# Optimization experiments

Measured on AMD Instinct MI355X. Metric: run time of the kernel, lower is better.

## Reference

```python
import jax, jax.numpy as jnp
import numpy as np

N, E, D, H, B = 10000, 160000, 128, 1, 4
SLOPE = 0.01  # negative_slope from DeepQNet default


def gat_layer(x, node_state, src, dst, W, att_src, att_dst, Wns, bns, bias):
    # x: [N,D] or [B,N,D]; node_state: [B,N,1]
    xs = x + node_state @ Wns + bns              # [B,N,D]
    Bx, Nn = xs.shape[0], xs.shape[1]
    h = (xs @ W).reshape(Bx, Nn, H, D)           # [B,N,H,C]
    a_src = (h * att_src).sum(-1)                # [B,N,H]
    a_dst = (h * att_dst).sum(-1)                # [B,N,H]
    ae = a_src[:, src] + a_dst[:, dst]           # [B,Etot,H]
    ae = jnp.where(ae > 0, ae, SLOPE * ae)       # leaky_relu
    ae_t = jnp.moveaxis(ae, 1, 0)                # [Etot,B,H]
    m = jax.ops.segment_max(ae_t, dst, num_segments=Nn)   # [N,B,H]
    e = jnp.exp(ae_t - m[dst])
    s = jax.ops.segment_sum(e, dst, num_segments=Nn)
    alpha = e / s[dst]                           # [Etot,B,H]
    h_e = jnp.moveaxis(h, 1, 0)                  # [N,B,H,C]
    msg = alpha[..., None] * h_e[src]            # [Etot,B,H,C]
    out = jax.ops.segment_sum(msg, dst, num_segments=Nn)  # [N,B,H,C]
    out = jnp.moveaxis(out, 0, 1).mean(2) + bias # concat=False -> head mean
    return jax.nn.relu(out)


def setup_inputs() -> dict:
    key = jax.random.key(0)
    ks = jax.random.split(key, 16)
    edges = jax.random.randint(ks[0], (2, E), 0, N)
    loop = jnp.arange(N)
    edge_index = jnp.concatenate([edges, jnp.stack([loop, loop])], axis=1)  # add_self_loops
    state = jax.random.uniform(ks[1], (B, N), dtype=jnp.float32)
    strucEmb = jax.random.normal(ks[2], (N, D), dtype=jnp.float32) * 0.1
    s = 0.05
    return {
        "state": state,
        "strucEmb": strucEmb,
        "edge_index": edge_index,
        "gat_W": jax.random.normal(ks[3], (3, D, H * D), dtype=jnp.float32) * s,
        "gat_att_src": jax.random.normal(ks[4], (3, H, D), dtype=jnp.float32) * s,
        "gat_att_dst": jax.random.normal(ks[5], (3, H, D), dtype=jnp.float32) * s,
        "gat_Wns": jax.random.normal(ks[6], (3, 1, D), dtype=jnp.float32) * s,
        "gat_bns": jnp.zeros((3, D), jnp.float32),
        "gat_bias": jnp.zeros((3, D), jnp.float32),
        "W1": jax.random.normal(ks[7], (D, D), dtype=jnp.float32) * s,
        "b1": jnp.zeros((D,), jnp.float32),
        "W2": jax.random.normal(ks[8], (D, D), dtype=jnp.float32) * s,
        "b2": jnp.zeros((D,), jnp.float32),
        "W3": jax.random.normal(ks[9], (2 * D, 1), dtype=jnp.float32) * s,
        "b3": jnp.zeros((1,), jnp.float32),
    }


def reference(state, strucEmb, edge_index, gat_W, gat_att_src, gat_att_dst,
              gat_Wns, gat_bns, gat_bias, W1, b1, W2, b2, W3, b3):
    src, dst = edge_index[0], edge_index[1]
    rs = state.reshape(state.shape[0], N, 1)     # [B,N,1]
    x = strucEmb
    for l in range(3):
        x = gat_layer(x, rs, src, dst, gat_W[l], gat_att_src[l], gat_att_dst[l],
                      gat_Wns[l], gat_bns[l], gat_bias[l])
    state_emb = x.sum(1)                         # [B,D]
    beta_state = state_emb @ W1 + b1             # [B,D]
    beta_action = x @ W2 + b2                    # [B,N,D]  (is_for_learn=True path)
    expand_state = jnp.broadcast_to(beta_state[:, None, :], beta_action.shape)
    out = jax.nn.relu(jnp.concatenate([expand_state, beta_action], axis=2))
    return out @ W3 + b3                         # [B,N,1]
```

## Files before the change

kernel.cpp:

```cpp
#include <hip/hip_runtime.h>
#include <math.h>

#define N_NODES 10000
#define B_SZ 4
#define SLOPE 0.01f
#define BN (B_SZ * N_NODES)
#define PADK 136

typedef __attribute__((ext_vector_type(8))) short short8;
typedef __attribute__((ext_vector_type(4))) float float4v;

__device__ __forceinline__ unsigned short f2bf(float f) {
    unsigned u = __builtin_bit_cast(unsigned, f);
    u += 0x7fffu + ((u >> 16) & 1u);
    return (unsigned short)(u >> 16);
}
__device__ __forceinline__ float bf2f(unsigned short s) {
    unsigned u = ((unsigned)s) << 16;
    return __builtin_bit_cast(float, u);
}


__global__ __launch_bounds__(256) void init_kernel(int* deg, int* cursor, float* state_emb) {
    int i = blockIdx.x * 256 + threadIdx.x;
    if (i < N_NODES) { deg[i] = 0; cursor[i] = 0; }
    if (i < B_SZ * 128) state_emb[i] = 0.f;
}

__global__ __launch_bounds__(256) void hist_kernel(const int* __restrict__ dst, int Etot, int* deg) {
    int e = blockIdx.x * 256 + threadIdx.x;
    if (e < Etot) atomicAdd(&deg[dst[e]], 1);
}

__global__ __launch_bounds__(1024) void scan_kernel(const int* __restrict__ deg, int* __restrict__ rowOff) {
    __shared__ int wsum[16];
    int tid = threadIdx.x;
    int lane = tid & 63, wid = tid >> 6;
    int base = tid * 10;
    int v[10]; int tot = 0;
#pragma unroll
    for (int j = 0; j < 10; j++) {
        int idx = base + j;
        int d = (idx < N_NODES) ? deg[idx] : 0;
        tot += d; v[j] = tot;
    }
    int incl = tot;
    for (int off = 1; off < 64; off <<= 1) {
        int t = __shfl_up(incl, off, 64);
        if (lane >= off) incl += t;
    }
    if (lane == 63) wsum[wid] = incl;
    __syncthreads();
    if (wid == 0) {
        int wv = (lane < 16) ? wsum[lane] : 0;
        for (int off = 1; off < 16; off <<= 1) {
            int t = __shfl_up(wv, off, 64);
            if (lane >= off) wv += t;
        }
        if (lane < 16) wsum[lane] = wv;
    }
    __syncthreads();
    int waveoff = (wid > 0) ? wsum[wid - 1] : 0;
    int excl = waveoff + incl - tot;
    if (tid == 0) rowOff[0] = 0;
#pragma unroll
    for (int j = 0; j < 10; j++) {
        int idx = base + j;
        if (idx < N_NODES) rowOff[idx + 1] = excl + v[j];
    }
}

__global__ __launch_bounds__(256) void scatter_kernel(const int* __restrict__ dst, int Etot,
                                                      const int* __restrict__ rowOff,
                                                      int* cursor, int* __restrict__ edgeLst) {
    int e = blockIdx.x * 256 + threadIdx.x;
    if (e < Etot) {
        int d = dst[e];
        int pos = rowOff[d] + atomicAdd(&cursor[d], 1);
        edgeLst[pos] = e;
    }
}


__global__ __launch_bounds__(256) void wconv_kernel(const float* __restrict__ gatW,
                                                    const float* __restrict__ W2,
                                                    unsigned short* __restrict__ whi,
                                                    unsigned short* __restrict__ wlo) {
    int w = blockIdx.y;
    int i = blockIdx.x * 256 + threadIdx.x;
    int k = i >> 7, c = i & 127;
    const float* src = (w < 3) ? (gatW + (size_t)w * 16384) : W2;
    float v = src[k * 128 + c];
    unsigned short h = f2bf(v);
    whi[w * 16384 + c * 128 + k] = h;
    wlo[w * 16384 + c * 128 + k] = f2bf(v - bf2f(h));
}


__global__ __launch_bounds__(256) void prep0_kernel(const float* __restrict__ strucEmb,
                                                    const float* __restrict__ state,
                                                    const float* __restrict__ Wns0,
                                                    const float* __restrict__ bns0,
                                                    unsigned short* __restrict__ XS) {
    int idx = blockIdx.x * 256 + threadIdx.x;
    int g = idx >> 7, d = idx & 127;
    int n = g >> 2, b = g & 3;
    float v = strucEmb[(size_t)n * 128 + d] + state[b * N_NODES + n] * Wns0[d] + bns0[d];
    XS[idx] = f2bf(v);
}


__global__ __launch_bounds__(256) void gemm_att_mfma(
    const unsigned short* __restrict__ XS,
    const unsigned short* __restrict__ WThi, const unsigned short* __restrict__ WTlo,
    const float* __restrict__ attS, const float* __restrict__ attD,
    unsigned short* __restrict__ Hout, float* __restrict__ aSrcP, float* __restrict__ aDstP)
{
    __shared__ __align__(16) unsigned short sCus[64 * PADK];
    __shared__ float sAs[128], sAd[128];
    __shared__ float sPart[64 * 8];

    int tid = threadIdx.x;
    int g0 = blockIdx.x * 64;
    int w = tid >> 6, lane = tid & 63;
    int quad = lane >> 4, mcol = lane & 15;

    if (tid < 128) { sAs[tid] = attS[tid]; sAd[tid] = attD[tid]; }

    short8 Bh[4][2], Bl[4][2];
#pragma unroll
    for (int kc = 0; kc < 4; kc++)
#pragma unroll
        for (int nt = 0; nt < 2; nt++) {
            int col = w * 32 + nt * 16 + mcol;
            Bh[kc][nt] = *(const short8*)(WThi + col * 128 + kc * 32 + quad * 8);
            Bl[kc][nt] = *(const short8*)(WTlo + col * 128 + kc * 32 + quad * 8);
        }
    short8 Af[4][4];
#pragma unroll
    for (int mt = 0; mt < 4; mt++)
#pragma unroll
        for (int kc = 0; kc < 4; kc++)
            Af[mt][kc] = *(const short8*)(XS + (size_t)(g0 + mt * 16 + mcol) * 128 + kc * 32 + quad * 8);

    float4v acc[4][2];
#pragma unroll
    for (int mt = 0; mt < 4; mt++)
#pragma unroll
        for (int nt = 0; nt < 2; nt++) acc[mt][nt] = (float4v){0.f, 0.f, 0.f, 0.f};

#pragma unroll
    for (int kc = 0; kc < 4; kc++)
#pragma unroll
        for (int mt = 0; mt < 4; mt++)
#pragma unroll
            for (int nt = 0; nt < 2; nt++) {
                acc[mt][nt] = __builtin_amdgcn_mfma_f32_16x16x32_bf16(Af[mt][kc], Bh[kc][nt], acc[mt][nt], 0, 0, 0);
                acc[mt][nt] = __builtin_amdgcn_mfma_f32_16x16x32_bf16(Af[mt][kc], Bl[kc][nt], acc[mt][nt], 0, 0, 0);
            }

    __syncthreads();

    float pp[16], pd[16];
#pragma unroll
    for (int r16 = 0; r16 < 16; r16++) { pp[r16] = 0.f; pd[r16] = 0.f; }
#pragma unroll
    for (int mt = 0; mt < 4; mt++)
#pragma unroll
        for (int nt = 0; nt < 2; nt++)
#pragma unroll
            for (int reg = 0; reg < 4; reg++) {
                int row = mt * 16 + quad * 4 + reg;
                int col = w * 32 + nt * 16 + mcol;
                float v = acc[mt][nt][reg];
                sCus[row * PADK + col] = f2bf(v);
                pp[mt * 4 + reg] += v * sAs[col];
                pd[mt * 4 + reg] += v * sAd[col];
            }
#pragma unroll
    for (int off = 1; off < 16; off <<= 1)
#pragma unroll
        for (int r16 = 0; r16 < 16; r16++) {
            pp[r16] += __shfl_xor(pp[r16], off);
            pd[r16] += __shfl_xor(pd[r16], off);
        }
    if (mcol == 0) {
#pragma unroll
        for (int r16 = 0; r16 < 16; r16++) {
            int row = (r16 >> 2) * 16 + quad * 4 + (r16 & 3);
            sPart[row * 8 + w * 2 + 0] = pp[r16];
            sPart[row * 8 + w * 2 + 1] = pd[r16];
        }
    }
    __syncthreads();

    for (int i = tid; i < 64 * 16; i += 256) {
        int r = i >> 4, c8 = i & 15;
        uint4 u = *(uint4*)(sCus + r * PADK + c8 * 8);
        *(uint4*)(Hout + (size_t)(g0 + r) * 128 + c8 * 8) = u;
    }
    if (tid < 64) {
        float s0 = sPart[tid * 8] + sPart[tid * 8 + 2] + sPart[tid * 8 + 4] + sPart[tid * 8 + 6];
        float s1 = sPart[tid * 8 + 1] + sPart[tid * 8 + 3] + sPart[tid * 8 + 5] + sPart[tid * 8 + 7];
        aSrcP[g0 + tid] = s0;
        aDstP[g0 + tid] = s1;
    }
}


__global__ __launch_bounds__(256) void sm_agg_kernel(
    const int* __restrict__ rowOff, const int* __restrict__ edgeLst,
    const int* __restrict__ srcArr,
    const float* __restrict__ aSrcP, const float* __restrict__ aDstP,
    const unsigned short* __restrict__ H,
    const float* __restrict__ bias,
    const float* __restrict__ state, const float* __restrict__ wnsN,
    const float* __restrict__ bnsN, int addNext,
    unsigned short* __restrict__ Xout)
{
    __shared__ int sSrc[64];
    __shared__ float sAe[64 * 4];
    int n = blockIdx.x;
    int start = rowOff[n], end = rowOff[n + 1];
    int cnt = end - start;
    int tid = threadIdx.x;
    int b = tid >> 6, t = tid & 63;
    float adst = aDstP[n * 4 + b];
    const unsigned int* Hu = (const unsigned int*)H;

    float accx = 0.f, accy = 0.f, inv = 0.f;

    if (cnt <= 64) {
        float ae = -1e30f;
        if (t < cnt) {
            int e = edgeLst[start + t];
            int sn = srcArr[e];
            if (b == 0) sSrc[t] = sn;
            float v = aSrcP[sn * 4 + b] + adst;
            ae = v > 0.f ? v : SLOPE * v;
            sAe[t * 4 + b] = ae;
        }
        float m = ae;
        m = fmaxf(m, __shfl_xor(m, 1));  m = fmaxf(m, __shfl_xor(m, 2));
        m = fmaxf(m, __shfl_xor(m, 4));  m = fmaxf(m, __shfl_xor(m, 8));
        m = fmaxf(m, __shfl_xor(m, 16)); m = fmaxf(m, __shfl_xor(m, 32));
        __syncthreads();
        float s = 0.f;
        int j = 0;
        for (; j + 4 <= cnt; j += 4) {
            float a0 = __expf(sAe[j * 4 + b] - m),       a1 = __expf(sAe[(j + 1) * 4 + b] - m);
            float a2 = __expf(sAe[(j + 2) * 4 + b] - m), a3 = __expf(sAe[(j + 3) * 4 + b] - m);
            int s0 = sSrc[j], s1 = sSrc[j + 1], s2 = sSrc[j + 2], s3 = sSrc[j + 3];
            s += a0 + a1 + a2 + a3;
            unsigned int h0 = Hu[(size_t)(s0 * 4 + b) * 64 + t];
            unsigned int h1 = Hu[(size_t)(s1 * 4 + b) * 64 + t];
            unsigned int h2 = Hu[(size_t)(s2 * 4 + b) * 64 + t];
            unsigned int h3 = Hu[(size_t)(s3 * 4 + b) * 64 + t];
            accx += a0 * __builtin_bit_cast(float, h0 << 16) + a1 * __builtin_bit_cast(float, h1 << 16)
                  + a2 * __builtin_bit_cast(float, h2 << 16) + a3 * __builtin_bit_cast(float, h3 << 16);
            accy += a0 * __builtin_bit_cast(float, h0 & 0xffff0000u) + a1 * __builtin_bit_cast(float, h1 & 0xffff0000u)
                  + a2 * __builtin_bit_cast(float, h2 & 0xffff0000u) + a3 * __builtin_bit_cast(float, h3 & 0xffff0000u);
        }
        for (; j < cnt; j++) {
            float a0 = __expf(sAe[j * 4 + b] - m);
            int s0 = sSrc[j];
            s += a0;
            unsigned int h0 = Hu[(size_t)(s0 * 4 + b) * 64 + t];
            accx += a0 * __builtin_bit_cast(float, h0 << 16);
            accy += a0 * __builtin_bit_cast(float, h0 & 0xffff0000u);
        }
        inv = 1.f / s;
    } else {
        float m = -1e30f;
        for (int i = start + t; i < end; i += 64) {
            int sn = srcArr[edgeLst[i]];
            float v = aSrcP[sn * 4 + b] + adst;
            m = fmaxf(m, v > 0.f ? v : SLOPE * v);
        }
        m = fmaxf(m, __shfl_xor(m, 1));  m = fmaxf(m, __shfl_xor(m, 2));
        m = fmaxf(m, __shfl_xor(m, 4));  m = fmaxf(m, __shfl_xor(m, 8));
        m = fmaxf(m, __shfl_xor(m, 16)); m = fmaxf(m, __shfl_xor(m, 32));
        float s = 0.f;
        for (int i = start + t; i < end; i += 64) {
            int sn = srcArr[edgeLst[i]];
            float v = aSrcP[sn * 4 + b] + adst;
            float ae = v > 0.f ? v : SLOPE * v;
            s += __expf(ae - m);
        }
        s += __shfl_xor(s, 1);  s += __shfl_xor(s, 2);  s += __shfl_xor(s, 4);
        s += __shfl_xor(s, 8);  s += __shfl_xor(s, 16); s += __shfl_xor(s, 32);
        for (int c0 = start; c0 < end; c0 += 64) {
            int c = min(64, end - c0);
            if (t < c) {
                int e = edgeLst[c0 + t];
                int sn = srcArr[e];
                if (b == 0) sSrc[t] = sn;
                float v = aSrcP[sn * 4 + b] + adst;
                float ae = v > 0.f ? v : SLOPE * v;
                sAe[t * 4 + b] = __expf(ae - m);
            }
            __syncthreads();
            for (int j = 0; j < c; j++) {
                float a0 = sAe[j * 4 + b];
                int s0 = sSrc[j];
                unsigned int h0 = Hu[(size_t)(s0 * 4 + b) * 64 + t];
                accx += a0 * __builtin_bit_cast(float, h0 << 16);
                accy += a0 * __builtin_bit_cast(float, h0 & 0xffff0000u);
            }
            __syncthreads();
        }
        inv = 1.f / s;
    }

    float ox = accx * inv + bias[2 * t];
    float oy = accy * inv + bias[2 * t + 1];
    ox = ox > 0.f ? ox : 0.f;
    oy = oy > 0.f ? oy : 0.f;
    if (addNext) {
        float st = state[b * N_NODES + n];
        ox += st * wnsN[2 * t]     + bnsN[2 * t];
        oy += st * wnsN[2 * t + 1] + bnsN[2 * t + 1];
    }
    unsigned px = f2bf(ox), py = f2bf(oy);
    ((unsigned*)Xout)[(size_t)(n * 4 + b) * 64 + t] = (py << 16) | px;
}


__global__ __launch_bounds__(128) void sum_nodes_kernel(const unsigned short* __restrict__ X, float* state_emb) {
    int cx = blockIdx.x, b = blockIdx.y, d = threadIdx.x;
    int n0 = cx * 157, n1 = n0 + 157;
    if (n1 > N_NODES) n1 = N_NODES;
    float acc = 0.f;
    for (int n = n0; n < n1; n++) acc += bf2f(X[(size_t)(n * 4 + b) * 128 + d]);
    atomicAdd(&state_emb[b * 128 + d], acc);
}

__global__ __launch_bounds__(512) void beta_state_kernel(
    const float* __restrict__ state_emb, const float* __restrict__ W1,
    const float* __restrict__ b1, const float* __restrict__ W3, float* c1)
{
    __shared__ float sm[512];
    int tid = threadIdx.x;
    int b = tid >> 7, d = tid & 127;
    float acc = b1[d];
    for (int k = 0; k < 128; k++) acc += state_emb[b * 128 + k] * W1[k * 128 + d];
    float v = acc > 0.f ? acc : 0.f;
    sm[tid] = v * W3[d];
    __syncthreads();
    for (int s = 64; s > 0; s >>= 1) {
        if (d < s) sm[tid] += sm[tid + s];
        __syncthreads();
    }
    if (d == 0) c1[b] = sm[tid];
}


__global__ __launch_bounds__(256) void final_mfma(
    const unsigned short* __restrict__ X,
    const unsigned short* __restrict__ WThi, const unsigned short* __restrict__ WTlo,
    const float* __restrict__ b2, const float* __restrict__ W3,
    const float* __restrict__ b3, const float* __restrict__ c1,
    float* __restrict__ out)
{
    __shared__ float sB2[128], sW3[128];
    __shared__ float sPart[64 * 4];

    int tid = threadIdx.x;
    int g0 = blockIdx.x * 64;
    int w = tid >> 6, lane = tid & 63;
    int quad = lane >> 4, mcol = lane & 15;

    if (tid < 128) { sB2[tid] = b2[tid]; sW3[tid] = W3[128 + tid]; }

    short8 Bh[4][2], Bl[4][2];
#pragma unroll
    for (int kc = 0; kc < 4; kc++)
#pragma unroll
        for (int nt = 0; nt < 2; nt++) {
            int col = w * 32 + nt * 16 + mcol;
            Bh[kc][nt] = *(const short8*)(WThi + col * 128 + kc * 32 + quad * 8);
            Bl[kc][nt] = *(const short8*)(WTlo + col * 128 + kc * 32 + quad * 8);
        }
    short8 Af[4][4];
#pragma unroll
    for (int mt = 0; mt < 4; mt++)
#pragma unroll
        for (int kc = 0; kc < 4; kc++)
            Af[mt][kc] = *(const short8*)(X + (size_t)(g0 + mt * 16 + mcol) * 128 + kc * 32 + quad * 8);

    float4v acc[4][2];
#pragma unroll
    for (int mt = 0; mt < 4; mt++)
#pragma unroll
        for (int nt = 0; nt < 2; nt++) acc[mt][nt] = (float4v){0.f, 0.f, 0.f, 0.f};

#pragma unroll
    for (int kc = 0; kc < 4; kc++)
#pragma unroll
        for (int mt = 0; mt < 4; mt++)
#pragma unroll
            for (int nt = 0; nt < 2; nt++) {
                acc[mt][nt] = __builtin_amdgcn_mfma_f32_16x16x32_bf16(Af[mt][kc], Bh[kc][nt], acc[mt][nt], 0, 0, 0);
                acc[mt][nt] = __builtin_amdgcn_mfma_f32_16x16x32_bf16(Af[mt][kc], Bl[kc][nt], acc[mt][nt], 0, 0, 0);
            }

    __syncthreads();

    float pp[16];
#pragma unroll
    for (int r16 = 0; r16 < 16; r16++) pp[r16] = 0.f;
#pragma unroll
    for (int mt = 0; mt < 4; mt++)
#pragma unroll
        for (int nt = 0; nt < 2; nt++)
#pragma unroll
            for (int reg = 0; reg < 4; reg++) {
                int col = w * 32 + nt * 16 + mcol;
                float v = acc[mt][nt][reg] + sB2[col];
                v = v > 0.f ? v : 0.f;
                pp[mt * 4 + reg] += v * sW3[col];
            }
#pragma unroll
    for (int off = 1; off < 16; off <<= 1)
#pragma unroll
        for (int r16 = 0; r16 < 16; r16++)
            pp[r16] += __shfl_xor(pp[r16], off);
    if (mcol == 0) {
#pragma unroll
        for (int r16 = 0; r16 < 16; r16++) {
            int row = (r16 >> 2) * 16 + quad * 4 + (r16 & 3);
            sPart[row * 4 + w] = pp[r16];
        }
    }
    __syncthreads();
    if (tid < 64) {
        float p = sPart[tid * 4] + sPart[tid * 4 + 1] + sPart[tid * 4 + 2] + sPart[tid * 4 + 3];
        int g = g0 + tid;
        out[(g & 3) * N_NODES + (g >> 2)] = p + c1[g & 3] + b3[0];
    }
}


extern "C" void kernel_launch(void* const* d_in, const int* in_sizes, int n_in,
                              void* d_out, int out_size, void* d_ws, size_t ws_size,
                              hipStream_t stream) {
    const float* state    = (const float*)d_in[0];
    const float* strucEmb = (const float*)d_in[1];
    const int*   edge_idx = (const int*)d_in[2];
    const float* gat_W    = (const float*)d_in[3];
    const float* gat_aS   = (const float*)d_in[4];
    const float* gat_aD   = (const float*)d_in[5];
    const float* gat_Wns  = (const float*)d_in[6];
    const float* gat_bns  = (const float*)d_in[7];
    const float* gat_bias = (const float*)d_in[8];
    const float* W1 = (const float*)d_in[9];
    const float* b1 = (const float*)d_in[10];
    const float* W2 = (const float*)d_in[11];
    const float* b2 = (const float*)d_in[12];
    const float* W3 = (const float*)d_in[13];
    const float* b3 = (const float*)d_in[14];
    float* out = (float*)d_out;

    int Etot = in_sizes[2] / 2;
    const int* srcArr = edge_idx;
    const int* dstArr = edge_idx + Etot;

    float* ws = (float*)d_ws;
    unsigned short* Xb = (unsigned short*)ws;
    unsigned short* Hb = (unsigned short*)(ws + 2560000);
    float* aSrcP       = ws + 5120000;
    float* aDstP       = ws + 5160000;
    float* state_emb   = ws + 5200000;
    float* c1          = ws + 5200512;
    unsigned short* whi = (unsigned short*)(ws + 5200516);
    unsigned short* wlo = whi + 4 * 16384;
    int*   iws         = (int*)(ws + 5200516 + 65536);
    int*   rowOff      = iws;
    int*   deg         = iws + 10001;
    int*   cursor      = deg + 10000;
    int*   edgeLst     = cursor + 10000;

    wconv_kernel<<<dim3(64, 4), 256, 0, stream>>>(gat_W, W2, whi, wlo);
    init_kernel<<<40, 256, 0, stream>>>(deg, cursor, state_emb);
    prep0_kernel<<<BN * 128 / 256, 256, 0, stream>>>(strucEmb, state, gat_Wns, gat_bns, Xb);
    hist_kernel<<<(Etot + 255) / 256, 256, 0, stream>>>(dstArr, Etot, deg);
    scan_kernel<<<1, 1024, 0, stream>>>(deg, rowOff);
    scatter_kernel<<<(Etot + 255) / 256, 256, 0, stream>>>(dstArr, Etot, rowOff, cursor, edgeLst);

    for (int l = 0; l < 3; l++) {
        gemm_att_mfma<<<BN / 64, 256, 0, stream>>>(
            Xb, whi + (size_t)l * 16384, wlo + (size_t)l * 16384,
            gat_aS + l * 128, gat_aD + l * 128, Hb, aSrcP, aDstP);
        sm_agg_kernel<<<N_NODES, 256, 0, stream>>>(
            rowOff, edgeLst, srcArr, aSrcP, aDstP, Hb, gat_bias + l * 128,
            state, gat_Wns + (l + 1 < 3 ? (l + 1) * 128 : 0),
            gat_bns + (l + 1 < 3 ? (l + 1) * 128 : 0), (l < 2) ? 1 : 0, Xb);
    }

    sum_nodes_kernel<<<dim3(64, B_SZ), 128, 0, stream>>>(Xb, state_emb);
    beta_state_kernel<<<1, 512, 0, stream>>>(state_emb, W1, b1, W3, c1);
    final_mfma<<<BN / 64, 256, 0, stream>>>(Xb, whi + 3 * 16384, wlo + 3 * 16384,
                                            b2, W3, b3, c1, out);
}
```

Measured before the change: 339.8 us.

## Merge setup kernels, store src in CSR, restructure aggregation and fold beta_state into final

Three setup kernels (weight conversion, init, layer-0 prep) are merged into one launch, and the CSR scatter now stores source node ids directly, removing an indirection in aggregation. The small-degree aggregation path normalizes alphas before accumulation and has each half-wave handle alternate edges with 8-byte loads, combined by a cross-half shuffle. The GEMM kernels loop over the hi and lo weight terms with per-kc A loads to reduce register pressure. The beta_state kernel is folded into final_mfma, so every block recomputes the small W1 product redundantly in exchange for one fewer launch.

```diff
diff --git a/kernel.cpp b/kernel.cpp
--- a/kernel.cpp
+++ b/kernel.cpp
@@ -19,13 +19,41 @@
     unsigned u = ((unsigned)s) << 16;
     return __builtin_bit_cast(float, u);
 }
-
-
-__global__ __launch_bounds__(256) void init_kernel(int* deg, int* cursor, float* state_emb) {
-    int i = blockIdx.x * 256 + threadIdx.x;
-    if (i < N_NODES) { deg[i] = 0; cursor[i] = 0; }
-    if (i < B_SZ * 128) state_emb[i] = 0.f;
-}
+__device__ __forceinline__ float bflo(unsigned u) { return __builtin_bit_cast(float, u << 16); }
+__device__ __forceinline__ float bfhi(unsigned u) { return __builtin_bit_cast(float, u & 0xffff0000u); }
+
+
+__global__ __launch_bounds__(256) void setup_kernel(
+    const float* __restrict__ strucEmb, const float* __restrict__ state,
+    const float* __restrict__ Wns0, const float* __restrict__ bns0,
+    const float* __restrict__ gatW, const float* __restrict__ W2,
+    unsigned short* __restrict__ XS,
+    unsigned short* __restrict__ whi, unsigned short* __restrict__ wlo,
+    int* deg, int* cursor, float* state_emb)
+{
+    int bx = blockIdx.x, tid = threadIdx.x;
+    if (bx < 20000) {
+        int idx = bx * 256 + tid;
+        int g = idx >> 7, d = idx & 127;
+        int n = g >> 2, b = g & 3;
+        float v = strucEmb[(size_t)n * 128 + d] + state[b * N_NODES + n] * Wns0[d] + bns0[d];
+        XS[idx] = f2bf(v);
+    } else if (bx < 20256) {
+        int i = (bx - 20000) * 256 + tid;
+        int w = i >> 14, rem = i & 16383;
+        int k = rem >> 7, c = rem & 127;
+        const float* src = (w < 3) ? (gatW + (size_t)w * 16384) : W2;
+        float v = src[k * 128 + c];
+        unsigned short h = f2bf(v);
+        whi[w * 16384 + c * 128 + k] = h;
+        wlo[w * 16384 + c * 128 + k] = f2bf(v - bf2f(h));
+    } else {
+        int i = (bx - 20256) * 256 + tid;
+        if (i < N_NODES) { deg[i] = 0; cursor[i] = 0; }
+        if (i < 512) state_emb[i] = 0.f;
+    }
+}
+
 
 __global__ __launch_bounds__(256) void hist_kernel(const int* __restrict__ dst, int Etot, int* deg) {
     int e = blockIdx.x * 256 + threadIdx.x;
@@ -70,43 +98,15 @@
     }
 }
 
-__global__ __launch_bounds__(256) void scatter_kernel(const int* __restrict__ dst, int Etot,
-                                                      const int* __restrict__ rowOff,
-                                                      int* cursor, int* __restrict__ edgeLst) {
+__global__ __launch_bounds__(256) void scatter_kernel(const int* __restrict__ src, const int* __restrict__ dst,
+                                                      int Etot, const int* __restrict__ rowOff,
+                                                      int* cursor, int* __restrict__ srcLst) {
     int e = blockIdx.x * 256 + threadIdx.x;
     if (e < Etot) {
         int d = dst[e];
         int pos = rowOff[d] + atomicAdd(&cursor[d], 1);
-        edgeLst[pos] = e;
-    }
-}
-
-
-__global__ __launch_bounds__(256) void wconv_kernel(const float* __restrict__ gatW,
-                                                    const float* __restrict__ W2,
-                                                    unsigned short* __restrict__ whi,
-                                                    unsigned short* __restrict__ wlo) {
-    int w = blockIdx.y;
-    int i = blockIdx.x * 256 + threadIdx.x;
-    int k = i >> 7, c = i & 127;
-    const float* src = (w < 3) ? (gatW + (size_t)w * 16384) : W2;
-    float v = src[k * 128 + c];
-    unsigned short h = f2bf(v);
-    whi[w * 16384 + c * 128 + k] = h;
-    wlo[w * 16384 + c * 128 + k] = f2bf(v - bf2f(h));
-}
-
-
-__global__ __launch_bounds__(256) void prep0_kernel(const float* __restrict__ strucEmb,
-                                                    const float* __restrict__ state,
-                                                    const float* __restrict__ Wns0,
-                                                    const float* __restrict__ bns0,
-                                                    unsigned short* __restrict__ XS) {
-    int idx = blockIdx.x * 256 + threadIdx.x;
-    int g = idx >> 7, d = idx & 127;
-    int n = g >> 2, b = g & 3;
-    float v = strucEmb[(size_t)n * 128 + d] + state[b * N_NODES + n] * Wns0[d] + bns0[d];
-    XS[idx] = f2bf(v);
+        srcLst[pos] = src[e];
+    }
 }
 
 
@@ -127,37 +127,34 @@
 
     if (tid < 128) { sAs[tid] = attS[tid]; sAd[tid] = attD[tid]; }
 
-    short8 Bh[4][2], Bl[4][2];
-#pragma unroll
-    for (int kc = 0; kc < 4; kc++)
-#pragma unroll
-        for (int nt = 0; nt < 2; nt++) {
-            int col = w * 32 + nt * 16 + mcol;
-            Bh[kc][nt] = *(const short8*)(WThi + col * 128 + kc * 32 + quad * 8);
-            Bl[kc][nt] = *(const short8*)(WTlo + col * 128 + kc * 32 + quad * 8);
-        }
-    short8 Af[4][4];
+    float4v acc[4][2];
 #pragma unroll
     for (int mt = 0; mt < 4; mt++)
 #pragma unroll
+        for (int nt = 0; nt < 2; nt++) acc[mt][nt] = (float4v){0.f, 0.f, 0.f, 0.f};
+
+#pragma unroll 1
+    for (int term = 0; term < 2; term++) {
+        const unsigned short* WT = term ? WTlo : WThi;
+        short8 Bf[4][2];
+#pragma unroll
         for (int kc = 0; kc < 4; kc++)
-            Af[mt][kc] = *(const short8*)(XS + (size_t)(g0 + mt * 16 + mcol) * 128 + kc * 32 + quad * 8);
-
-    float4v acc[4][2];
-#pragma unroll
-    for (int mt = 0; mt < 4; mt++)
-#pragma unroll
-        for (int nt = 0; nt < 2; nt++) acc[mt][nt] = (float4v){0.f, 0.f, 0.f, 0.f};
-
-#pragma unroll
-    for (int kc = 0; kc < 4; kc++)
-#pragma unroll
-        for (int mt = 0; mt < 4; mt++)
-#pragma unroll
-            for (int nt = 0; nt < 2; nt++) {
-                acc[mt][nt] = __builtin_amdgcn_mfma_f32_16x16x32_bf16(Af[mt][kc], Bh[kc][nt], acc[mt][nt], 0, 0, 0);
-                acc[mt][nt] = __builtin_amdgcn_mfma_f32_16x16x32_bf16(Af[mt][kc], Bl[kc][nt], acc[mt][nt], 0, 0, 0);
-            }
+#pragma unroll
+            for (int nt = 0; nt < 2; nt++)
+                Bf[kc][nt] = *(const short8*)(WT + (w * 32 + nt * 16 + mcol) * 128 + kc * 32 + quad * 8);
+#pragma unroll
+        for (int kc = 0; kc < 4; kc++) {
+            short8 Aa[4];
+#pragma unroll
+            for (int mt = 0; mt < 4; mt++)
+                Aa[mt] = *(const short8*)(XS + (size_t)(g0 + mt * 16 + mcol) * 128 + kc * 32 + quad * 8);
+#pragma unroll
+            for (int mt = 0; mt < 4; mt++)
+#pragma unroll
+                for (int nt = 0; nt < 2; nt++)
+                    acc[mt][nt] = __builtin_amdgcn_mfma_f32_16x16x32_bf16(Aa[mt], Bf[kc][nt], acc[mt][nt], 0, 0, 0);
+        }
+    }
 
     __syncthreads();
 
@@ -209,8 +206,7 @@
 
 
 __global__ __launch_bounds__(256) void sm_agg_kernel(
-    const int* __restrict__ rowOff, const int* __restrict__ edgeLst,
-    const int* __restrict__ srcArr,
+    const int* __restrict__ rowOff, const int* __restrict__ srcLst,
     const float* __restrict__ aSrcP, const float* __restrict__ aDstP,
     const unsigned short* __restrict__ H,
     const float* __restrict__ bias,
@@ -226,54 +222,77 @@
     int tid = threadIdx.x;
     int b = tid >> 6, t = tid & 63;
     float adst = aDstP[n * 4 + b];
-    const unsigned int* Hu = (const unsigned int*)H;
-
-    float accx = 0.f, accy = 0.f, inv = 0.f;
+    const unsigned* Hu = (const unsigned*)H;
 
     if (cnt <= 64) {
         float ae = -1e30f;
         if (t < cnt) {
-            int e = edgeLst[start + t];
-            int sn = srcArr[e];
+            int sn = srcLst[start + t];
             if (b == 0) sSrc[t] = sn;
             float v = aSrcP[sn * 4 + b] + adst;
             ae = v > 0.f ? v : SLOPE * v;
-            sAe[t * 4 + b] = ae;
         }
         float m = ae;
         m = fmaxf(m, __shfl_xor(m, 1));  m = fmaxf(m, __shfl_xor(m, 2));
         m = fmaxf(m, __shfl_xor(m, 4));  m = fmaxf(m, __shfl_xor(m, 8));
         m = fmaxf(m, __shfl_xor(m, 16)); m = fmaxf(m, __shfl_xor(m, 32));
+        float e = (t < cnt) ? __expf(ae - m) : 0.f;
+        float s = e;
+        s += __shfl_xor(s, 1);  s += __shfl_xor(s, 2);  s += __shfl_xor(s, 4);
+        s += __shfl_xor(s, 8);  s += __shfl_xor(s, 16); s += __shfl_xor(s, 32);
+        float inv = 1.f / s;
+        if (t < cnt) sAe[t * 4 + b] = e * inv;
         __syncthreads();
-        float s = 0.f;
+
+        int half = t >> 5, cc = t & 31;
+        float a0 = 0.f, a1 = 0.f, a2 = 0.f, a3 = 0.f;
         int j = 0;
-        for (; j + 4 <= cnt; j += 4) {
-            float a0 = __expf(sAe[j * 4 + b] - m),       a1 = __expf(sAe[(j + 1) * 4 + b] - m);
-            float a2 = __expf(sAe[(j + 2) * 4 + b] - m), a3 = __expf(sAe[(j + 3) * 4 + b] - m);
-            int s0 = sSrc[j], s1 = sSrc[j + 1], s2 = sSrc[j + 2], s3 = sSrc[j + 3];
-            s += a0 + a1 + a2 + a3;
-            unsigned int h0 = Hu[(size_t)(s0 * 4 + b) * 64 + t];
-            unsigned int h1 = Hu[(size_t)(s1 * 4 + b) * 64 + t];
-            unsigned int h2 = Hu[(size_t)(s2 * 4 + b) * 64 + t];
-            unsigned int h3 = Hu[(size_t)(s3 * 4 + b) * 64 + t];
-            accx += a0 * __builtin_bit_cast(float, h0 << 16) + a1 * __builtin_bit_cast(float, h1 << 16)
-                  + a2 * __builtin_bit_cast(float, h2 << 16) + a3 * __builtin_bit_cast(float, h3 << 16);
-            accy += a0 * __builtin_bit_cast(float, h0 & 0xffff0000u) + a1 * __builtin_bit_cast(float, h1 & 0xffff0000u)
-                  + a2 * __builtin_bit_cast(float, h2 & 0xffff0000u) + a3 * __builtin_bit_cast(float, h3 & 0xffff0000u);
-        }
-        for (; j < cnt; j++) {
-            float a0 = __expf(sAe[j * 4 + b] - m);
-            int s0 = sSrc[j];
-            s += a0;
-            unsigned int h0 = Hu[(size_t)(s0 * 4 + b) * 64 + t];
-            accx += a0 * __builtin_bit_cast(float, h0 << 16);
-            accy += a0 * __builtin_bit_cast(float, h0 & 0xffff0000u);
-        }
-        inv = 1.f / s;
+        for (; j + 8 <= cnt; j += 8) {
+            int j0 = j + half, j1 = j + 2 + half, j2 = j + 4 + half, j3 = j + 6 + half;
+            int s0 = sSrc[j0], s1 = sSrc[j1], s2 = sSrc[j2], s3 = sSrc[j3];
+            uint2 h0 = *(const uint2*)(Hu + (size_t)(s0 * 4 + b) * 64 + cc * 2);
+            uint2 h1 = *(const uint2*)(Hu + (size_t)(s1 * 4 + b) * 64 + cc * 2);
+            uint2 h2 = *(const uint2*)(Hu + (size_t)(s2 * 4 + b) * 64 + cc * 2);
+            uint2 h3 = *(const uint2*)(Hu + (size_t)(s3 * 4 + b) * 64 + cc * 2);
+            float al0 = sAe[j0 * 4 + b], al1 = sAe[j1 * 4 + b];
+            float al2 = sAe[j2 * 4 + b], al3 = sAe[j3 * 4 + b];
+            a0 += al0 * bflo(h0.x) + al1 * bflo(h1.x) + al2 * bflo(h2.x) + al3 * bflo(h3.x);
+            a1 += al0 * bfhi(h0.x) + al1 * bfhi(h1.x) + al2 * bfhi(h2.x) + al3 * bfhi(h3.x);
+            a2 += al0 * bflo(h0.y) + al1 * bflo(h1.y) + al2 * bflo(h2.y) + al3 * bflo(h3.y);
+            a3 += al0 * bfhi(h0.y) + al1 * bfhi(h1.y) + al2 * bfhi(h2.y) + al3 * bfhi(h3.y);
+        }
+        for (; j < cnt; j += 2) {
+            int jj = j + half;
+            bool valid = jj < cnt;
+            int sj = sSrc[valid ? jj : j];
+            float al = valid ? sAe[jj * 4 + b] : 0.f;
+            uint2 hv = *(const uint2*)(Hu + (size_t)(sj * 4 + b) * 64 + cc * 2);
+            a0 += al * bflo(hv.x); a1 += al * bfhi(hv.x);
+            a2 += al * bflo(hv.y); a3 += al * bfhi(hv.y);
+        }
+        a0 += __shfl_xor(a0, 32); a1 += __shfl_xor(a1, 32);
+        a2 += __shfl_xor(a2, 32); a3 += __shfl_xor(a3, 32);
+        if (half == 0) {
+            int d0 = cc * 4;
+            float o0 = fmaxf(a0 + bias[d0],     0.f);
+            float o1 = fmaxf(a1 + bias[d0 + 1], 0.f);
+            float o2 = fmaxf(a2 + bias[d0 + 2], 0.f);
+            float o3 = fmaxf(a3 + bias[d0 + 3], 0.f);
+            if (addNext) {
+                float st = state[b * N_NODES + n];
+                o0 += st * wnsN[d0]     + bnsN[d0];
+                o1 += st * wnsN[d0 + 1] + bnsN[d0 + 1];
+                o2 += st * wnsN[d0 + 2] + bnsN[d0 + 2];
+                o3 += st * wnsN[d0 + 3] + bnsN[d0 + 3];
+            }
+            unsigned wlo2 = (unsigned)f2bf(o0) | ((unsigned)f2bf(o1) << 16);
+            unsigned whi2 = (unsigned)f2bf(o2) | ((unsigned)f2bf(o3) << 16);
+            *(uint2*)((unsigned*)Xout + (size_t)(n * 4 + b) * 64 + cc * 2) = make_uint2(wlo2, whi2);
+        }
     } else {
         float m = -1e30f;
         for (int i = start + t; i < end; i += 64) {
-            int sn = srcArr[edgeLst[i]];
+            int sn = srcLst[i];
             float v = aSrcP[sn * 4 + b] + adst;
             m = fmaxf(m, v > 0.f ? v : SLOPE * v);
         }
@@ -282,47 +301,43 @@
         m = fmaxf(m, __shfl_xor(m, 16)); m = fmaxf(m, __shfl_xor(m, 32));
         float s = 0.f;
         for (int i = start + t; i < end; i += 64) {
-            int sn = srcArr[edgeLst[i]];
+            int sn = srcLst[i];
             float v = aSrcP[sn * 4 + b] + adst;
-            float ae = v > 0.f ? v : SLOPE * v;
-            s += __expf(ae - m);
+            float ae2 = v > 0.f ? v : SLOPE * v;
+            s += __expf(ae2 - m);
         }
         s += __shfl_xor(s, 1);  s += __shfl_xor(s, 2);  s += __shfl_xor(s, 4);
         s += __shfl_xor(s, 8);  s += __shfl_xor(s, 16); s += __shfl_xor(s, 32);
+        float inv = 1.f / s;
+        float accx = 0.f, accy = 0.f;
         for (int c0 = start; c0 < end; c0 += 64) {
             int c = min(64, end - c0);
             if (t < c) {
-                int e = edgeLst[c0 + t];
-                int sn = srcArr[e];
+                int sn = srcLst[c0 + t];
                 if (b == 0) sSrc[t] = sn;
                 float v = aSrcP[sn * 4 + b] + adst;
-                float ae = v > 0.f ? v : SLOPE * v;
-                sAe[t * 4 + b] = __expf(ae - m);
+                float ae2 = v > 0.f ? v : SLOPE * v;
+                sAe[t * 4 + b] = __expf(ae2 - m);
             }
             __syncthreads();
             for (int j = 0; j < c; j++) {
                 float a0 = sAe[j * 4 + b];
-                int s0 = sSrc[j];
-                unsigned int h0 = Hu[(size_t)(s0 * 4 + b) * 64 + t];
-                accx += a0 * __builtin_bit_cast(float, h0 << 16);
-                accy += a0 * __builtin_bit_cast(float, h0 & 0xffff0000u);
+                unsigned h0 = Hu[(size_t)(sSrc[j] * 4 + b) * 64 + t];
+                accx += a0 * bflo(h0);
+                accy += a0 * bfhi(h0);
             }
             __syncthreads();
         }
-        inv = 1.f / s;
-    }
-
-    float ox = accx * inv + bias[2 * t];
-    float oy = accy * inv + bias[2 * t + 1];
-    ox = ox > 0.f ? ox : 0.f;
-    oy = oy > 0.f ? oy : 0.f;
-    if (addNext) {
-        float st = state[b * N_NODES + n];
-        ox += st * wnsN[2 * t]     + bnsN[2 * t];
-        oy += st * wnsN[2 * t + 1] + bnsN[2 * t + 1];
-    }
-    unsigned px = f2bf(ox), py = f2bf(oy);
-    ((unsigned*)Xout)[(size_t)(n * 4 + b) * 64 + t] = (py << 16) | px;
+        float ox = fmaxf(accx * inv + bias[2 * t], 0.f);
+        float oy = fmaxf(accy * inv + bias[2 * t + 1], 0.f);
+        if (addNext) {
+            float st = state[b * N_NODES + n];
+            ox += st * wnsN[2 * t]     + bnsN[2 * t];
+            oy += st * wnsN[2 * t + 1] + bnsN[2 * t + 1];
+        }
+        ((unsigned*)Xout)[(size_t)(n * 4 + b) * 64 + t] =
+            (unsigned)f2bf(ox) | ((unsigned)f2bf(oy) << 16);
+    }
 }
 
 
@@ -335,35 +350,19 @@
     atomicAdd(&state_emb[b * 128 + d], acc);
 }
 
-__global__ __launch_bounds__(512) void beta_state_kernel(
-    const float* __restrict__ state_emb, const float* __restrict__ W1,
-    const float* __restrict__ b1, const float* __restrict__ W3, float* c1)
-{
-    __shared__ float sm[512];
-    int tid = threadIdx.x;
-    int b = tid >> 7, d = tid & 127;
-    float acc = b1[d];
-    for (int k = 0; k < 128; k++) acc += state_emb[b * 128 + k] * W1[k * 128 + d];
-    float v = acc > 0.f ? acc : 0.f;
-    sm[tid] = v * W3[d];
-    __syncthreads();
-    for (int s = 64; s > 0; s >>= 1) {
-        if (d < s) sm[tid] += sm[tid + s];
-        __syncthreads();
-    }
-    if (d == 0) c1[b] = sm[tid];
-}
-
 
 __global__ __launch_bounds__(256) void final_mfma(
     const unsigned short* __restrict__ X,
     const unsigned short* __restrict__ WThi, const unsigned short* __restrict__ WTlo,
     const float* __restrict__ b2, const float* __restrict__ W3,
-    const float* __restrict__ b3, const float* __restrict__ c1,
+    const float* __restrict__ b3,
+    const float* __restrict__ state_emb, const float* __restrict__ W1,
+    const float* __restrict__ b1,
     float* __restrict__ out)
 {
     __shared__ float sB2[128], sW3[128];
     __shared__ float sPart[64 * 4];
+    __shared__ float sC1p[8], sC1[4];
 
     int tid = threadIdx.x;
     int g0 = blockIdx.x * 64;
@@ -372,39 +371,59 @@
 
     if (tid < 128) { sB2[tid] = b2[tid]; sW3[tid] = W3[128 + tid]; }
 
-    short8 Bh[4][2], Bl[4][2];
-#pragma unroll
-    for (int kc = 0; kc < 4; kc++)
-#pragma unroll
-        for (int nt = 0; nt < 2; nt++) {
-            int col = w * 32 + nt * 16 + mcol;
-            Bh[kc][nt] = *(const short8*)(WThi + col * 128 + kc * 32 + quad * 8);
-            Bl[kc][nt] = *(const short8*)(WTlo + col * 128 + kc * 32 + quad * 8);
-        }
-    short8 Af[4][4];
+    {
+        int d = tid & 127;
+        int bh = tid >> 7;
+        float p0 = b1[d], p1 = b1[d];
+        for (int k = 0; k < 128; k++) {
+            float wv = W1[k * 128 + d];
+            p0 += state_emb[bh * 128 + k] * wv;
+            p1 += state_emb[(bh + 2) * 128 + k] * wv;
+        }
+        float w3d = W3[d];
+        p0 = fmaxf(p0, 0.f) * w3d;
+        p1 = fmaxf(p1, 0.f) * w3d;
+#pragma unroll
+        for (int off = 1; off < 64; off <<= 1) {
+            p0 += __shfl_xor(p0, off);
+            p1 += __shfl_xor(p1, off);
+        }
+        if (lane == 0) { sC1p[w * 2 + 0] = p0; sC1p[w * 2 + 1] = p1; }
+    }
+    __syncthreads();
+    if (tid == 0) {
+        sC1[0] = sC1p[0] + sC1p[2];  sC1[2] = sC1p[1] + sC1p[3];
+        sC1[1] = sC1p[4] + sC1p[6];  sC1[3] = sC1p[5] + sC1p[7];
+    }
+
+    float4v acc[4][2];
 #pragma unroll
     for (int mt = 0; mt < 4; mt++)
 #pragma unroll
+        for (int nt = 0; nt < 2; nt++) acc[mt][nt] = (float4v){0.f, 0.f, 0.f, 0.f};
+
+#pragma unroll 1
+    for (int term = 0; term < 2; term++) {
+        const unsigned short* WT = term ? WTlo : WThi;
+        short8 Bf[4][2];
+#pragma unroll
         for (int kc = 0; kc < 4; kc++)
-            Af[mt][kc] = *(const short8*)(X + (size_t)(g0 + mt * 16 + mcol) * 128 + kc * 32 + quad * 8);
-
-    float4v acc[4][2];
-#pragma unroll
-    for (int mt = 0; mt < 4; mt++)
-#pragma unroll
-        for (int nt = 0; nt < 2; nt++) acc[mt][nt] = (float4v){0.f, 0.f, 0.f, 0.f};
-
-#pragma unroll
-    for (int kc = 0; kc < 4; kc++)
-#pragma unroll
-        for (int mt = 0; mt < 4; mt++)
-#pragma unroll
-            for (int nt = 0; nt < 2; nt++) {
-                acc[mt][nt] = __builtin_amdgcn_mfma_f32_16x16x32_bf16(Af[mt][kc], Bh[kc][nt], acc[mt][nt], 0, 0, 0);
-                acc[mt][nt] = __builtin_amdgcn_mfma_f32_16x16x32_bf16(Af[mt][kc], Bl[kc][nt], acc[mt][nt], 0, 0, 0);
-            }
-
-    __syncthreads();
+#pragma unroll
+            for (int nt = 0; nt < 2; nt++)
+                Bf[kc][nt] = *(const short8*)(WT + (w * 32 + nt * 16 + mcol) * 128 + kc * 32 + quad * 8);
+#pragma unroll
+        for (int kc = 0; kc < 4; kc++) {
+            short8 Aa[4];
+#pragma unroll
+            for (int mt = 0; mt < 4; mt++)
+                Aa[mt] = *(const short8*)(X + (size_t)(g0 + mt * 16 + mcol) * 128 + kc * 32 + quad * 8);
+#pragma unroll
+            for (int mt = 0; mt < 4; mt++)
+#pragma unroll
+                for (int nt = 0; nt < 2; nt++)
+                    acc[mt][nt] = __builtin_amdgcn_mfma_f32_16x16x32_bf16(Aa[mt], Bf[kc][nt], acc[mt][nt], 0, 0, 0);
+        }
+    }
 
     float pp[16];
 #pragma unroll
@@ -436,7 +455,7 @@
     if (tid < 64) {
         float p = sPart[tid * 4] + sPart[tid * 4 + 1] + sPart[tid * 4 + 2] + sPart[tid * 4 + 3];
         int g = g0 + tid;
-        out[(g & 3) * N_NODES + (g >> 2)] = p + c1[g & 3] + b3[0];
+        out[(g & 3) * N_NODES + (g >> 2)] = p + sC1[g & 3] + b3[0];
     }
 }
 
@@ -471,34 +490,31 @@
     float* aSrcP       = ws + 5120000;
     float* aDstP       = ws + 5160000;
     float* state_emb   = ws + 5200000;
-    float* c1          = ws + 5200512;
     unsigned short* whi = (unsigned short*)(ws + 5200516);
     unsigned short* wlo = whi + 4 * 16384;
     int*   iws         = (int*)(ws + 5200516 + 65536);
     int*   rowOff      = iws;
     int*   deg         = iws + 10001;
     int*   cursor      = deg + 10000;
-    int*   edgeLst     = cursor + 10000;
-
-    wconv_kernel<<<dim3(64, 4), 256, 0, stream>>>(gat_W, W2, whi, wlo);
-    init_kernel<<<40, 256, 0, stream>>>(deg, cursor, state_emb);
-    prep0_kernel<<<BN * 128 / 256, 256, 0, stream>>>(strucEmb, state, gat_Wns, gat_bns, Xb);
+    int*   srcLst      = cursor + 10000;
+
+    setup_kernel<<<20296, 256, 0, stream>>>(strucEmb, state, gat_Wns, gat_bns,
+                                            gat_W, W2, Xb, whi, wlo, deg, cursor, state_emb);
     hist_kernel<<<(Etot + 255) / 256, 256, 0, stream>>>(dstArr, Etot, deg);
     scan_kernel<<<1, 1024, 0, stream>>>(deg, rowOff);
-    scatter_kernel<<<(Etot + 255) / 256, 256, 0, stream>>>(dstArr, Etot, rowOff, cursor, edgeLst);
+    scatter_kernel<<<(Etot + 255) / 256, 256, 0, stream>>>(srcArr, dstArr, Etot, rowOff, cursor, srcLst);
 
     for (int l = 0; l < 3; l++) {
         gemm_att_mfma<<<BN / 64, 256, 0, stream>>>(
             Xb, whi + (size_t)l * 16384, wlo + (size_t)l * 16384,
             gat_aS + l * 128, gat_aD + l * 128, Hb, aSrcP, aDstP);
         sm_agg_kernel<<<N_NODES, 256, 0, stream>>>(
-            rowOff, edgeLst, srcArr, aSrcP, aDstP, Hb, gat_bias + l * 128,
+            rowOff, srcLst, aSrcP, aDstP, Hb, gat_bias + l * 128,
             state, gat_Wns + (l + 1 < 3 ? (l + 1) * 128 : 0),
             gat_bns + (l + 1 < 3 ? (l + 1) * 128 : 0), (l < 2) ? 1 : 0, Xb);
     }
 
     sum_nodes_kernel<<<dim3(64, B_SZ), 128, 0, stream>>>(Xb, state_emb);
-    beta_state_kernel<<<1, 512, 0, stream>>>(state_emb, W1, b1, W3, c1);
     final_mfma<<<BN / 64, 256, 0, stream>>>(Xb, whi + 3 * 16384, wlo + 3 * 16384,
-                                            b2, W3, b3, c1, out);
-}
+                                            b2, W3, b3, state_emb, W1, b1, out);
+}
```

Measured after the change: 337.3 us. No clear change (-0.7%).
